# Performance work log

Measured on AMD Instinct MI355X. Metric: run time of the kernel, lower is better.

Reference implementation:

```python
import jax, jax.numpy as jnp
import numpy as np

B, T, C = 2, 2048, 2048
N_HEAD, KV_HEADS = 16, 4
HEAD_DIM = C // N_HEAD  # 128
EPS = 1e-6


def setup_inputs() -> dict:
    key = jax.random.key(0)
    ks = jax.random.split(key, 3)
    x = jax.random.normal(ks[0], (B, T, C), dtype=jnp.float32)
    qkv_out = (N_HEAD + 2 * KV_HEADS) * HEAD_DIM  # 3072
    w_qkv = jax.random.normal(ks[1], (qkv_out, C), dtype=jnp.float32) * 0.02
    w_proj = jax.random.normal(ks[2], (C, C), dtype=jnp.float32) * 0.02
    q_norm_w = jnp.ones((HEAD_DIM,), dtype=jnp.float32)
    k_norm_w = jnp.ones((HEAD_DIM,), dtype=jnp.float32)
    # RoPE frequencies: theta = 10000^{-2i/d}, angles = pos * theta
    inv_freq = 1.0 / (10000.0 ** (np.arange(0, HEAD_DIM, 2, dtype=np.float32) / HEAD_DIM))
    angles = np.arange(T, dtype=np.float32)[:, None] * inv_freq[None, :]  # [T, 64]
    freqs_cos = jnp.asarray(np.cos(angles), dtype=jnp.float32)
    freqs_sin = jnp.asarray(np.sin(angles), dtype=jnp.float32)
    return {"x": x, "w_qkv": w_qkv, "w_proj": w_proj,
            "q_norm_w": q_norm_w, "k_norm_w": k_norm_w,
            "freqs_cos": freqs_cos, "freqs_sin": freqs_sin}


def _rope(t, cos, sin):
    # t: [B, H, T, D]; interpret last dim as D/2 complex pairs (a, b)
    a = t[..., 0::2]
    b = t[..., 1::2]
    oa = a * cos - b * sin
    ob = a * sin + b * cos
    return jnp.stack([oa, ob], axis=-1).reshape(t.shape)


def _rmsnorm(t, w, eps=EPS):
    rms = jnp.sqrt(jnp.mean(t * t, axis=-1, keepdims=True) + eps)
    return w * (t / rms)


def reference(x, w_qkv, w_proj, q_norm_w, k_norm_w, freqs_cos, freqs_sin):
    b, t, c = x.shape
    hd = HEAD_DIM
    qkv = x @ w_qkv.T  # [B, T, 3072]
    q_size = N_HEAD * hd
    kv_size = KV_HEADS * hd
    q = qkv[..., :q_size].reshape(b, t, N_HEAD, hd).transpose(0, 2, 1, 3)
    k = qkv[..., q_size:q_size + kv_size].reshape(b, t, KV_HEADS, hd).transpose(0, 2, 1, 3)
    v = qkv[..., q_size + kv_size:].reshape(b, t, KV_HEADS, hd).transpose(0, 2, 1, 3)
    # repeat_interleave KV heads to match query heads (GQA)
    rep = N_HEAD // KV_HEADS
    k = jnp.repeat(k, rep, axis=1)
    v = jnp.repeat(v, rep, axis=1)
    # RoPE (applied after repeat, matching the torch code order)
    cos = freqs_cos[:t][None, None, :, :]
    sin = freqs_sin[:t][None, None, :, :]
    q = _rope(q, cos, sin)
    k = _rope(k, cos, sin)
    # QK RMSNorm per head_dim
    q = _rmsnorm(q, q_norm_w)
    k = _rmsnorm(k, k_norm_w)
    # causal SDPA
    scores = jnp.einsum('bhqd,bhkd->bhqk', q, k) / jnp.sqrt(jnp.float32(hd))
    causal = jnp.tril(jnp.ones((t, t), dtype=bool))
    scores = jnp.where(causal[None, None], scores, jnp.finfo(scores.dtype).min)
    att = jax.nn.softmax(scores, axis=-1)
    y = jnp.einsum('bhqk,bhkd->bhqd', att, v)
    y = y.transpose(0, 2, 1, 3).reshape(b, t, c)
    return y @ w_proj.T
```

## Files before the change

kernel.cpp:

```cpp
#include <hip/hip_runtime.h>
#include <hip/hip_bf16.h>

#define B_    2
#define T_    2048
#define C_    2048
#define NH_   16
#define KVH_  4
#define HD_   128
#define QKV_  3072
#define M_    4096

typedef float  floatx4 __attribute__((ext_vector_type(4)));
typedef __bf16 bf16x8  __attribute__((ext_vector_type(8)));
typedef __bf16 bf16x4  __attribute__((ext_vector_type(4)));
typedef __bf16 bf16x2  __attribute__((ext_vector_type(2)));

typedef const __attribute__((address_space(1))) void* gas_t;
typedef __attribute__((address_space(3))) void*       las_t;
__device__ __forceinline__ void gl_lds16(const void* g, void* l) {
  __builtin_amdgcn_global_load_lds((gas_t)g, (las_t)l, 16, 0, 0);
}

__global__ __launch_bounds__(256) void cvt_bf16(const float* __restrict__ src,
                                                __bf16* __restrict__ dst, int n4) {
  int i = blockIdx.x * blockDim.x + threadIdx.x;
  if (i < n4) {
    float4 f = ((const float4*)src)[i];
    bf16x4 o = { (__bf16)f.x, (__bf16)f.y, (__bf16)f.z, (__bf16)f.w };
    ((bf16x4*)dst)[i] = o;
  }
}

__global__ __launch_bounds__(256) void gemm_bt(const __bf16* __restrict__ A,
                                               const __bf16* __restrict__ Bm,
                                               float* __restrict__ Cc,
                                               int N, int K) {
  __shared__ __align__(16) __bf16 As[128 * 32];
  __shared__ __align__(16) __bf16 Bs[128 * 32];
  const int tid  = threadIdx.x;
  const int wid  = tid >> 6, lane = tid & 63, quad = lane >> 4, r16 = lane & 15;
  const int bm   = blockIdx.y * 128, bn = blockIdx.x * 128;
  const int wm   = (wid >> 1) * 64, wn = (wid & 1) * 64;
  const int srow = wid * 16 + (lane >> 2);
  const int scol = (lane & 3) * 8;
  const __bf16* aptr = A  + (size_t)(bm + srow) * K + scol;
  const __bf16* bptr = Bm + (size_t)(bn + srow) * K + scol;
  __bf16* ldsA0 = &As[wid * 512];
  __bf16* ldsA1 = &As[2048 + wid * 512];
  __bf16* ldsB0 = &Bs[wid * 512];
  __bf16* ldsB1 = &Bs[2048 + wid * 512];
  const size_t rowskip = (size_t)64 * K;

  floatx4 acc[4][4];
  #pragma unroll
  for (int i = 0; i < 4; i++)
    #pragma unroll
    for (int j = 0; j < 4; j++) acc[i][j] = (floatx4){0.f, 0.f, 0.f, 0.f};

  for (int k0 = 0; k0 < K; k0 += 32) {
    gl_lds16(aptr + k0,           ldsA0);
    gl_lds16(aptr + rowskip + k0, ldsA1);
    gl_lds16(bptr + k0,           ldsB0);
    gl_lds16(bptr + rowskip + k0, ldsB1);
    __syncthreads();

    bf16x8 af[4], bfr[4];
    #pragma unroll
    for (int i = 0; i < 4; i++) af[i]  = *(const bf16x8*)&As[(wm + i * 16 + r16) * 32 + quad * 8];
    #pragma unroll
    for (int j = 0; j < 4; j++) bfr[j] = *(const bf16x8*)&Bs[(wn + j * 16 + r16) * 32 + quad * 8];

    #pragma unroll
    for (int i = 0; i < 4; i++)
      #pragma unroll
      for (int j = 0; j < 4; j++)
        acc[i][j] = __builtin_amdgcn_mfma_f32_16x16x32_bf16(af[i], bfr[j], acc[i][j], 0, 0, 0);
    __syncthreads();
  }

  #pragma unroll
  for (int i = 0; i < 4; i++) {
    #pragma unroll
    for (int reg = 0; reg < 4; reg++) {
      int row = bm + wm + i * 16 + quad * 4 + reg;
      float* crow = Cc + (size_t)row * N + bn + wn;
      #pragma unroll
      for (int j = 0; j < 4; j++) crow[j * 16 + r16] = acc[i][j][reg];
    }
  }
}

__global__ __launch_bounds__(256) void rope_norm(const float* __restrict__ qkv,
                                                 const float* __restrict__ qw,
                                                 const float* __restrict__ kw,
                                                 const float* __restrict__ fc,
                                                 const float* __restrict__ fs,
                                                 __bf16* __restrict__ qn,
                                                 __bf16* __restrict__ kn) {
  const int tid  = threadIdx.x;
  const int wid  = tid >> 6, lane = tid & 63;
  const int row  = blockIdx.x * 4 + wid;
  const int b    = row >> 11, t = row & (T_ - 1);
  const float cs = fc[t * 64 + lane], sn = fs[t * 64 + lane];
  const float* base = qkv + (size_t)row * QKV_;

  #pragma unroll 2
  for (int h = 0; h < NH_; h++) {
    float2 ab = *(const float2*)(base + h * HD_ + 2 * lane);
    float oa = ab.x * cs - ab.y * sn;
    float ob = ab.x * sn + ab.y * cs;
    float ss = oa * oa + ob * ob;
    #pragma unroll
    for (int off = 32; off; off >>= 1) ss += __shfl_xor(ss, off);
    float rinv = rsqrtf(ss * (1.0f / HD_) + 1e-6f);
    bf16x2 o = { (__bf16)(oa * rinv * qw[2 * lane]), (__bf16)(ob * rinv * qw[2 * lane + 1]) };
    *(bf16x2*)&qn[(size_t)((b * NH_ + h) * T_ + t) * HD_ + 2 * lane] = o;
  }
  #pragma unroll 2
  for (int h = 0; h < KVH_; h++) {
    float2 ab = *(const float2*)(base + C_ + h * HD_ + 2 * lane);
    float oa = ab.x * cs - ab.y * sn;
    float ob = ab.x * sn + ab.y * cs;
    float ss = oa * oa + ob * ob;
    #pragma unroll
    for (int off = 32; off; off >>= 1) ss += __shfl_xor(ss, off);
    float rinv = rsqrtf(ss * (1.0f / HD_) + 1e-6f);
    bf16x2 o = { (__bf16)(oa * rinv * kw[2 * lane]), (__bf16)(ob * rinv * kw[2 * lane + 1]) };
    *(bf16x2*)&kn[(size_t)((b * KVH_ + h) * T_ + t) * HD_ + 2 * lane] = o;
  }
}

__global__ __launch_bounds__(256) void vtrans(const float* __restrict__ qkv,
                                              __bf16* __restrict__ vT) {
  __shared__ __bf16 L[64 * 68];
  const int tid = threadIdx.x;
  const int t0 = blockIdx.x * 64;
  const int d0 = blockIdx.y * 64;
  const int z  = blockIdx.z;
  const int b  = z >> 2, hk = z & 3;
  const int srcc = C_ + KVH_ * HD_ + hk * HD_ + d0;
  const int rr = tid >> 4, c4 = (tid & 15) * 4;
  #pragma unroll
  for (int i = 0; i < 4; i++) {
    int t = rr + i * 16;
    float4 f = *(const float4*)&qkv[(size_t)(b * T_ + t0 + t) * QKV_ + srcc + c4];
    bf16x4 o = { (__bf16)f.x, (__bf16)f.y, (__bf16)f.z, (__bf16)f.w };
    *(bf16x4*)&L[t * 68 + c4] = o;
  }
  __syncthreads();
  const int dr = tid >> 3, tc8 = (tid & 7) * 8;
  #pragma unroll
  for (int i = 0; i < 2; i++) {
    int d = dr + i * 32;
    bf16x8 ov;
    #pragma unroll
    for (int j = 0; j < 8; j++) ov[j] = L[(tc8 + j) * 68 + d];
    *(bf16x8*)&vT[(size_t)(z * HD_ + d0 + d) * T_ + t0 + tc8] = ov;
  }
}

__device__ __forceinline__ void kv_prefetch(const __bf16* kbase, const __bf16* vbase,
                                            int kt0, int wid, int lane,
                                            bf16x8 kreg[4], bf16x8 vreg[4]) {
  const int r4 = lane >> 2, c8 = (lane & 3) * 8;
  const __bf16* kg = kbase + (size_t)(kt0 + wid * 16 + r4) * HD_ + c8;
  #pragma unroll
  for (int cb = 0; cb < 4; cb++) kreg[cb] = *(const bf16x8*)(kg + cb * 32);
  #pragma unroll
  for (int s = 0; s < 2; s++) {
    const __bf16* vg = vbase + (size_t)((wid * 2 + s) * 16 + r4) * T_ + kt0 + c8;
    #pragma unroll
    for (int cb = 0; cb < 2; cb++) vreg[s * 2 + cb] = *(const bf16x8*)(vg + cb * 32);
  }
}

__device__ __forceinline__ void kv_commit(__bf16* Ks, __bf16* Vs, int wid, int lane,
                                          const bf16x8 kreg[4], const bf16x8 vreg[4]) {
  #pragma unroll
  for (int cb = 0; cb < 4; cb++)
    *(bf16x8*)(Ks + wid * 2048 + cb * 512 + lane * 8) = kreg[cb];
  #pragma unroll
  for (int s = 0; s < 2; s++)
    #pragma unroll
    for (int cb = 0; cb < 2; cb++)
      *(bf16x8*)(Vs + (wid * 2 + s) * 1024 + cb * 512 + lane * 8) = vreg[s * 2 + cb];
}

__global__ __launch_bounds__(256) void flash(const __bf16* __restrict__ q,
                                             const __bf16* __restrict__ k,
                                             const __bf16* __restrict__ vT,
                                             __bf16* __restrict__ y) {
  __shared__ __align__(16) __bf16 Ks[64 * 128];
  __shared__ __align__(16) __bf16 Vs[128 * 64];
  __shared__ __align__(16) __bf16 Ps[4][16 * 72];
  const int tid = threadIdx.x;
  const int wid = tid >> 6, lane = tid & 63, quad = lane >> 4, r16 = lane & 15;
  const int h = blockIdx.y, b = blockIdx.z;
  const int hk = h >> 2;
  const __bf16* kbase = k  + (size_t)(b * KVH_ + hk) * T_ * HD_;
  const __bf16* vbase = vT + (size_t)(b * KVH_ + hk) * HD_ * T_;
  __bf16* Pw = Ps[wid];
  const float sc = 0.08838834764831845f;
  const float NEG = -__builtin_inff();
  bf16x8 ones;
  #pragma unroll
  for (int i = 0; i < 8; i++) ones[i] = (__bf16)1.0f;

  #pragma unroll 1
  for (int pass = 0; pass < 2; ++pass) {
    const int qt = pass ? blockIdx.x : (31 - blockIdx.x);
    const int nt = qt + 1;
    const int r0 = qt * 64 + wid * 16;

    const __bf16* qrow = q + ((size_t)(b * NH_ + h) * T_ + r0 + r16) * HD_;
    bf16x8 qf[4];
    #pragma unroll
    for (int kb = 0; kb < 4; kb++) qf[kb] = *(const bf16x8*)&qrow[kb * 32 + quad * 8];

    floatx4 o[8], ol = (floatx4){0.f, 0.f, 0.f, 0.f};
    #pragma unroll
    for (int j = 0; j < 8; j++) o[j] = (floatx4){0.f, 0.f, 0.f, 0.f};
    float m_r[4] = {NEG, NEG, NEG, NEG};

    bf16x8 kreg[4], vreg[4];
    kv_prefetch(kbase, vbase, 0, wid, lane, kreg, vreg);

    #pragma unroll 1
    for (int it = 0; it < nt; ++it) {
      __syncthreads();
      kv_commit(Ks, Vs, wid, lane, kreg, vreg);
      __syncthreads();
      if (it + 1 < nt) kv_prefetch(kbase, vbase, (it + 1) * 64, wid, lane, kreg, vreg);

      const int kt0 = it * 64;
      floatx4 s[4];
      #pragma unroll
      for (int cb = 0; cb < 4; cb++) s[cb] = (floatx4){0.f, 0.f, 0.f, 0.f};
      #pragma unroll
      for (int kb = 0; kb < 4; kb++)
        #pragma unroll
        for (int cb = 0; cb < 4; cb++) {
          bf16x8 kf = *(const bf16x8*)&Ks[(cb * 4 + kb) * 512 + r16 * 32 + quad * 8];
          s[cb] = __builtin_amdgcn_mfma_f32_16x16x32_bf16(qf[kb], kf, s[cb], 0, 0, 0);
        }

      const bool last = (it == nt - 1);
      float alpha[4];
      #pragma unroll
      for (int reg = 0; reg < 4; reg++) {
        const int rowq = r0 + quad * 4 + reg;
        float v0 = s[0][reg] * sc, v1 = s[1][reg] * sc, v2 = s[2][reg] * sc, v3 = s[3][reg] * sc;
        if (last) {
          if (kt0 +      r16 > rowq) v0 = NEG;
          if (kt0 + 16 + r16 > rowq) v1 = NEG;
          if (kt0 + 32 + r16 > rowq) v2 = NEG;
          if (kt0 + 48 + r16 > rowq) v3 = NEG;
        }
        float mx = fmaxf(fmaxf(v0, v1), fmaxf(v2, v3));
        #pragma unroll
        for (int off = 8; off; off >>= 1) mx = fmaxf(mx, __shfl_xor(mx, off));
        float mnew = fmaxf(m_r[reg], mx);
        alpha[reg] = __expf(m_r[reg] - mnew);
        m_r[reg] = mnew;
        Pw[(quad * 4 + reg) * 72 +      r16] = (__bf16)__expf(v0 - mnew);
        Pw[(quad * 4 + reg) * 72 + 16 + r16] = (__bf16)__expf(v1 - mnew);
        Pw[(quad * 4 + reg) * 72 + 32 + r16] = (__bf16)__expf(v2 - mnew);
        Pw[(quad * 4 + reg) * 72 + 48 + r16] = (__bf16)__expf(v3 - mnew);
      }
      #pragma unroll
      for (int reg = 0; reg < 4; reg++) {
        ol[reg] *= alpha[reg];
        #pragma unroll
        for (int j = 0; j < 8; j++) o[j][reg] *= alpha[reg];
      }
      __asm__ volatile("" ::: "memory");
      bf16x8 pf0 = *(const bf16x8*)&Pw[r16 * 72 + quad * 8];
      bf16x8 pf1 = *(const bf16x8*)&Pw[r16 * 72 + 32 + quad * 8];
      ol = __builtin_amdgcn_mfma_f32_16x16x32_bf16(pf0, ones, ol, 0, 0, 0);
      ol = __builtin_amdgcn_mfma_f32_16x16x32_bf16(pf1, ones, ol, 0, 0, 0);
      #pragma unroll
      for (int j = 0; j < 8; j++) {
        bf16x8 vf0 = *(const bf16x8*)&Vs[(j * 2 + 0) * 512 + r16 * 32 + quad * 8];
        bf16x8 vf1 = *(const bf16x8*)&Vs[(j * 2 + 1) * 512 + r16 * 32 + quad * 8];
        o[j] = __builtin_amdgcn_mfma_f32_16x16x32_bf16(pf0, vf0, o[j], 0, 0, 0);
        o[j] = __builtin_amdgcn_mfma_f32_16x16x32_bf16(pf1, vf1, o[j], 0, 0, 0);
      }
    }

    #pragma unroll
    for (int reg = 0; reg < 4; reg++) {
      int trow = r0 + quad * 4 + reg;
      float inv = 1.0f / ol[reg];
      __bf16* yr = y + ((size_t)(b * T_) + trow) * C_ + h * HD_;
      #pragma unroll
      for (int j = 0; j < 8; j++) yr[j * 16 + r16] = (__bf16)(o[j][reg] * inv);
    }
  }
}

extern "C" void kernel_launch(void* const* d_in, const int* in_sizes, int n_in,
                              void* d_out, int out_size, void* d_ws, size_t ws_size,
                              hipStream_t stream) {
  const float* x     = (const float*)d_in[0];
  const float* wqkv  = (const float*)d_in[1];
  const float* wproj = (const float*)d_in[2];
  const float* qw    = (const float*)d_in[3];
  const float* kw    = (const float*)d_in[4];
  const float* fc    = (const float*)d_in[5];
  const float* fs    = (const float*)d_in[6];
  float* out = (float*)d_out;

  char* w = (char*)d_ws;
  __bf16* xb     = (__bf16*)w; w += (size_t)M_ * C_ * 2;
  __bf16* wqkvb  = (__bf16*)w; w += (size_t)QKV_ * C_ * 2;
  __bf16* wprojb = (__bf16*)w; w += (size_t)C_ * C_ * 2;
  float*  qkv    = (float*)w;  w += (size_t)M_ * QKV_ * 4;
  __bf16* qn     = (__bf16*)w; w += (size_t)B_ * NH_ * T_ * HD_ * 2;
  __bf16* kn     = (__bf16*)w; w += (size_t)B_ * KVH_ * T_ * HD_ * 2;
  __bf16* vT     = (__bf16*)w; w += (size_t)B_ * KVH_ * T_ * HD_ * 2;
  __bf16* ybf    = (__bf16*)w; w += (size_t)M_ * C_ * 2;

  cvt_bf16<<<M_ * C_ / 4 / 256, 256, 0, stream>>>(x, xb, M_ * C_ / 4);
  cvt_bf16<<<QKV_ * C_ / 4 / 256, 256, 0, stream>>>(wqkv, wqkvb, QKV_ * C_ / 4);
  cvt_bf16<<<C_ * C_ / 4 / 256, 256, 0, stream>>>(wproj, wprojb, C_ * C_ / 4);

  gemm_bt<<<dim3(QKV_ / 128, M_ / 128), 256, 0, stream>>>(xb, wqkvb, qkv, QKV_, C_);
  rope_norm<<<M_ / 4, 256, 0, stream>>>(qkv, qw, kw, fc, fs, qn, kn);
  vtrans<<<dim3(T_ / 64, HD_ / 64, B_ * KVH_), 256, 0, stream>>>(qkv, vT);
  flash<<<dim3(16, NH_, B_), 256, 0, stream>>>(qn, kn, vT, ybf);
  gemm_bt<<<dim3(C_ / 128, M_ / 128), 256, 0, stream>>>(ybf, wprojb, out, C_, C_);
}
```

Baseline: 362.1 us.

## Compute transposed scores in flash attention and pass P through registers

The QK^T MFMA now swaps its operands so each lane holds scores for a single query row across keys. Row max and row sum reduce with two cross-lane shuffles instead of a four-step butterfly per register. The softmax probabilities are packed to bf16 and redistributed with lane shuffles into the PV MFMA operand layout, which removes the per-wave LDS round trip for P and the ones-vector MFMA used for the row sum. The kernel also drops the two-pass pairing of a long and a short query tile per block and launches 32 blocks per head, one query tile each, which gives up the explicit causal load balancing.

```diff
diff --git a/kernel.cpp b/kernel.cpp
--- a/kernel.cpp
+++ b/kernel.cpp
@@ -19,6 +19,11 @@
 typedef __attribute__((address_space(3))) void*       las_t;
 __device__ __forceinline__ void gl_lds16(const void* g, void* l) {
   __builtin_amdgcn_global_load_lds((gas_t)g, (las_t)l, 16, 0, 0);
+}
+
+__device__ __forceinline__ int pack2(float a, float b) {
+  bf16x2 t = { (__bf16)a, (__bf16)b };
+  return __builtin_bit_cast(int, t);
 }
 
 __global__ __launch_bounds__(256) void cvt_bf16(const float* __restrict__ src,
@@ -192,109 +197,128 @@
                                              __bf16* __restrict__ y) {
   __shared__ __align__(16) __bf16 Ks[64 * 128];
   __shared__ __align__(16) __bf16 Vs[128 * 64];
-  __shared__ __align__(16) __bf16 Ps[4][16 * 72];
   const int tid = threadIdx.x;
   const int wid = tid >> 6, lane = tid & 63, quad = lane >> 4, r16 = lane & 15;
   const int h = blockIdx.y, b = blockIdx.z;
   const int hk = h >> 2;
   const __bf16* kbase = k  + (size_t)(b * KVH_ + hk) * T_ * HD_;
   const __bf16* vbase = vT + (size_t)(b * KVH_ + hk) * HD_ * T_;
-  __bf16* Pw = Ps[wid];
   const float sc = 0.08838834764831845f;
   const float NEG = -__builtin_inff();
-  bf16x8 ones;
-  #pragma unroll
-  for (int i = 0; i < 8; i++) ones[i] = (__bf16)1.0f;
+
+  const int qt = 31 - blockIdx.x;
+  const int nt = qt + 1;
+  const int r0 = qt * 64 + wid * 16;
+  const int rowq = r0 + r16;
+
+  const __bf16* qrow = q + ((size_t)(b * NH_ + h) * T_ + r0 + r16) * HD_;
+  bf16x8 qf[4];
+  #pragma unroll
+  for (int kb = 0; kb < 4; kb++) qf[kb] = *(const bf16x8*)&qrow[kb * 32 + quad * 8];
+
+  floatx4 o[8];
+  #pragma unroll
+  for (int j = 0; j < 8; j++) o[j] = (floatx4){0.f, 0.f, 0.f, 0.f};
+  float m_r = NEG, l_r = 0.f;
+
+  bf16x8 kreg[4], vreg[4];
+  kv_prefetch(kbase, vbase, 0, wid, lane, kreg, vreg);
 
   #pragma unroll 1
-  for (int pass = 0; pass < 2; ++pass) {
-    const int qt = pass ? blockIdx.x : (31 - blockIdx.x);
-    const int nt = qt + 1;
-    const int r0 = qt * 64 + wid * 16;
-
-    const __bf16* qrow = q + ((size_t)(b * NH_ + h) * T_ + r0 + r16) * HD_;
-    bf16x8 qf[4];
-    #pragma unroll
-    for (int kb = 0; kb < 4; kb++) qf[kb] = *(const bf16x8*)&qrow[kb * 32 + quad * 8];
-
-    floatx4 o[8], ol = (floatx4){0.f, 0.f, 0.f, 0.f};
-    #pragma unroll
-    for (int j = 0; j < 8; j++) o[j] = (floatx4){0.f, 0.f, 0.f, 0.f};
-    float m_r[4] = {NEG, NEG, NEG, NEG};
-
-    bf16x8 kreg[4], vreg[4];
-    kv_prefetch(kbase, vbase, 0, wid, lane, kreg, vreg);
-
-    #pragma unroll 1
-    for (int it = 0; it < nt; ++it) {
-      __syncthreads();
-      kv_commit(Ks, Vs, wid, lane, kreg, vreg);
-      __syncthreads();
-      if (it + 1 < nt) kv_prefetch(kbase, vbase, (it + 1) * 64, wid, lane, kreg, vreg);
-
-      const int kt0 = it * 64;
-      floatx4 s[4];
-      #pragma unroll
-      for (int cb = 0; cb < 4; cb++) s[cb] = (floatx4){0.f, 0.f, 0.f, 0.f};
-      #pragma unroll
-      for (int kb = 0; kb < 4; kb++)
-        #pragma unroll
-        for (int cb = 0; cb < 4; cb++) {
-          bf16x8 kf = *(const bf16x8*)&Ks[(cb * 4 + kb) * 512 + r16 * 32 + quad * 8];
-          s[cb] = __builtin_amdgcn_mfma_f32_16x16x32_bf16(qf[kb], kf, s[cb], 0, 0, 0);
-        }
-
-      const bool last = (it == nt - 1);
-      float alpha[4];
+  for (int it = 0; it < nt; ++it) {
+    __syncthreads();
+    kv_commit(Ks, Vs, wid, lane, kreg, vreg);
+    __syncthreads();
+    if (it + 1 < nt) kv_prefetch(kbase, vbase, (it + 1) * 64, wid, lane, kreg, vreg);
+
+    const int kt0 = it * 64;
+    floatx4 s[4];
+    #pragma unroll
+    for (int cb = 0; cb < 4; cb++) s[cb] = (floatx4){0.f, 0.f, 0.f, 0.f};
+    #pragma unroll
+    for (int kb = 0; kb < 4; kb++)
+      #pragma unroll
+      for (int cb = 0; cb < 4; cb++) {
+        bf16x8 kf = *(const bf16x8*)&Ks[(cb * 4 + kb) * 512 + r16 * 32 + quad * 8];
+        s[cb] = __builtin_amdgcn_mfma_f32_16x16x32_bf16(kf, qf[kb], s[cb], 0, 0, 0);
+      }
+
+    const bool last = (it == nt - 1);
+    float mx = NEG;
+    #pragma unroll
+    for (int cb = 0; cb < 4; cb++)
       #pragma unroll
       for (int reg = 0; reg < 4; reg++) {
-        const int rowq = r0 + quad * 4 + reg;
-        float v0 = s[0][reg] * sc, v1 = s[1][reg] * sc, v2 = s[2][reg] * sc, v3 = s[3][reg] * sc;
-        if (last) {
-          if (kt0 +      r16 > rowq) v0 = NEG;
-          if (kt0 + 16 + r16 > rowq) v1 = NEG;
-          if (kt0 + 32 + r16 > rowq) v2 = NEG;
-          if (kt0 + 48 + r16 > rowq) v3 = NEG;
-        }
-        float mx = fmaxf(fmaxf(v0, v1), fmaxf(v2, v3));
-        #pragma unroll
-        for (int off = 8; off; off >>= 1) mx = fmaxf(mx, __shfl_xor(mx, off));
-        float mnew = fmaxf(m_r[reg], mx);
-        alpha[reg] = __expf(m_r[reg] - mnew);
-        m_r[reg] = mnew;
-        Pw[(quad * 4 + reg) * 72 +      r16] = (__bf16)__expf(v0 - mnew);
-        Pw[(quad * 4 + reg) * 72 + 16 + r16] = (__bf16)__expf(v1 - mnew);
-        Pw[(quad * 4 + reg) * 72 + 32 + r16] = (__bf16)__expf(v2 - mnew);
-        Pw[(quad * 4 + reg) * 72 + 48 + r16] = (__bf16)__expf(v3 - mnew);
+        float vv = s[cb][reg] * sc;
+        if (last && (kt0 + cb * 16 + quad * 4 + reg > rowq)) vv = NEG;
+        s[cb][reg] = vv;
+        mx = fmaxf(mx, vv);
       }
+    mx = fmaxf(mx, __shfl_xor(mx, 16));
+    mx = fmaxf(mx, __shfl_xor(mx, 32));
+    const float mnew = fmaxf(m_r, mx);
+    const float alpha = __expf(m_r - mnew);
+    m_r = mnew;
+
+    float rs = 0.f;
+    #pragma unroll
+    for (int cb = 0; cb < 4; cb++)
       #pragma unroll
       for (int reg = 0; reg < 4; reg++) {
-        ol[reg] *= alpha[reg];
-        #pragma unroll
-        for (int j = 0; j < 8; j++) o[j][reg] *= alpha[reg];
+        float p = __expf(s[cb][reg] - mnew);
+        s[cb][reg] = p;
+        rs += p;
       }
-      __asm__ volatile("" ::: "memory");
-      bf16x8 pf0 = *(const bf16x8*)&Pw[r16 * 72 + quad * 8];
-      bf16x8 pf1 = *(const bf16x8*)&Pw[r16 * 72 + 32 + quad * 8];
-      ol = __builtin_amdgcn_mfma_f32_16x16x32_bf16(pf0, ones, ol, 0, 0, 0);
-      ol = __builtin_amdgcn_mfma_f32_16x16x32_bf16(pf1, ones, ol, 0, 0, 0);
+    rs += __shfl_xor(rs, 16);
+    rs += __shfl_xor(rs, 32);
+    l_r = l_r * alpha + rs;
+
+    int pk[4][2];
+    #pragma unroll
+    for (int cb = 0; cb < 4; cb++) {
+      pk[cb][0] = pack2(s[cb][0], s[cb][1]);
+      pk[cb][1] = pack2(s[cb][2], s[cb][3]);
+    }
+
+    float al[4];
+    #pragma unroll
+    for (int reg = 0; reg < 4; reg++) al[reg] = __shfl(alpha, quad * 4 + reg);
+    #pragma unroll
+    for (int reg = 0; reg < 4; reg++)
+      #pragma unroll
+      for (int j = 0; j < 8; j++) o[j][reg] *= al[reg];
+
+    const int srcA = ((quad & 1) << 5) + r16;
+    const int srcB = srcA + 16;
+    const bool hi = quad >= 2;
+    #pragma unroll
+    for (int half = 0; half < 2; half++) {
+      const int c0 = half * 2, c1 = half * 2 + 1;
+      int a0 = __shfl(pk[c0][0], srcA), b0 = __shfl(pk[c1][0], srcA);
+      int a1 = __shfl(pk[c0][1], srcA), b1 = __shfl(pk[c1][1], srcA);
+      int a2 = __shfl(pk[c0][0], srcB), b2 = __shfl(pk[c1][0], srcB);
+      int a3 = __shfl(pk[c0][1], srcB), b3 = __shfl(pk[c1][1], srcB);
+      union { int i[4]; bf16x8 v; } u;
+      u.i[0] = hi ? b0 : a0;
+      u.i[1] = hi ? b1 : a1;
+      u.i[2] = hi ? b2 : a2;
+      u.i[3] = hi ? b3 : a3;
       #pragma unroll
       for (int j = 0; j < 8; j++) {
-        bf16x8 vf0 = *(const bf16x8*)&Vs[(j * 2 + 0) * 512 + r16 * 32 + quad * 8];
-        bf16x8 vf1 = *(const bf16x8*)&Vs[(j * 2 + 1) * 512 + r16 * 32 + quad * 8];
-        o[j] = __builtin_amdgcn_mfma_f32_16x16x32_bf16(pf0, vf0, o[j], 0, 0, 0);
-        o[j] = __builtin_amdgcn_mfma_f32_16x16x32_bf16(pf1, vf1, o[j], 0, 0, 0);
+        bf16x8 vf = *(const bf16x8*)&Vs[(j * 2 + half) * 512 + r16 * 32 + quad * 8];
+        o[j] = __builtin_amdgcn_mfma_f32_16x16x32_bf16(u.v, vf, o[j], 0, 0, 0);
       }
     }
-
-    #pragma unroll
-    for (int reg = 0; reg < 4; reg++) {
-      int trow = r0 + quad * 4 + reg;
-      float inv = 1.0f / ol[reg];
-      __bf16* yr = y + ((size_t)(b * T_) + trow) * C_ + h * HD_;
-      #pragma unroll
-      for (int j = 0; j < 8; j++) yr[j * 16 + r16] = (__bf16)(o[j][reg] * inv);
-    }
+  }
+
+  #pragma unroll
+  for (int reg = 0; reg < 4; reg++) {
+    int trow = r0 + quad * 4 + reg;
+    float lf = __shfl(l_r, quad * 4 + reg);
+    float inv = 1.0f / lf;
+    __bf16* yr = y + ((size_t)(b * T_) + trow) * C_ + h * HD_;
+    #pragma unroll
+    for (int j = 0; j < 8; j++) yr[j * 16 + r16] = (__bf16)(o[j][reg] * inv);
   }
 }
 
@@ -327,6 +351,6 @@
   gemm_bt<<<dim3(QKV_ / 128, M_ / 128), 256, 0, stream>>>(xb, wqkvb, qkv, QKV_, C_);
   rope_norm<<<M_ / 4, 256, 0, stream>>>(qkv, qw, kw, fc, fs, qn, kn);
   vtrans<<<dim3(T_ / 64, HD_ / 64, B_ * KVH_), 256, 0, stream>>>(qkv, vT);
-  flash<<<dim3(16, NH_, B_), 256, 0, stream>>>(qn, kn, vT, ybf);
+  flash<<<dim3(32, NH_, B_), 256, 0, stream>>>(qn, kn, vT, ybf);
   gemm_bt<<<dim3(C_ / 128, M_ / 128), 256, 0, stream>>>(ybf, wprojb, out, C_, C_);
 }
```

New measurement: 423.5 us. +16.9%, slower.

## Enlarge flash query tile to 128 rows and double GEMM K-step

Applied to the files above, without the earlier changes.

The flash kernel now has each block handle a 128-row query tile, with each wave owning 32 rows as two 16-row subtiles, so every K/V tile loaded into LDS feeds twice as many MFMAs. The old two-pass balanced scheduling is replaced by a flat 512-block grid that launches the heaviest tiles first and skips fully masked tiles per wave. The GEMM now loads 64 K-columns per barrier pair instead of 32, halving synchronizations. The costs are higher register pressure in flash (launch bounds now ask for 2 blocks), possible warp idling on diagonal tiles, and more LDS use in the GEMM.

```diff
diff --git a/kernel.cpp b/kernel.cpp
--- a/kernel.cpp
+++ b/kernel.cpp
@@ -35,8 +35,8 @@
                                                const __bf16* __restrict__ Bm,
                                                float* __restrict__ Cc,
                                                int N, int K) {
-  __shared__ __align__(16) __bf16 As[128 * 32];
-  __shared__ __align__(16) __bf16 Bs[128 * 32];
+  __shared__ __align__(16) __bf16 As[2][128 * 32];
+  __shared__ __align__(16) __bf16 Bs[2][128 * 32];
   const int tid  = threadIdx.x;
   const int wid  = tid >> 6, lane = tid & 63, quad = lane >> 4, r16 = lane & 15;
   const int bm   = blockIdx.y * 128, bn = blockIdx.x * 128;
@@ -45,10 +45,6 @@
   const int scol = (lane & 3) * 8;
   const __bf16* aptr = A  + (size_t)(bm + srow) * K + scol;
   const __bf16* bptr = Bm + (size_t)(bn + srow) * K + scol;
-  __bf16* ldsA0 = &As[wid * 512];
-  __bf16* ldsA1 = &As[2048 + wid * 512];
-  __bf16* ldsB0 = &Bs[wid * 512];
-  __bf16* ldsB1 = &Bs[2048 + wid * 512];
   const size_t rowskip = (size_t)64 * K;
 
   floatx4 acc[4][4];
@@ -57,24 +53,29 @@
     #pragma unroll
     for (int j = 0; j < 4; j++) acc[i][j] = (floatx4){0.f, 0.f, 0.f, 0.f};
 
-  for (int k0 = 0; k0 < K; k0 += 32) {
-    gl_lds16(aptr + k0,           ldsA0);
-    gl_lds16(aptr + rowskip + k0, ldsA1);
-    gl_lds16(bptr + k0,           ldsB0);
-    gl_lds16(bptr + rowskip + k0, ldsB1);
+  for (int k0 = 0; k0 < K; k0 += 64) {
+    #pragma unroll
+    for (int hf = 0; hf < 2; hf++) {
+      gl_lds16(aptr + k0 + hf * 32,           &As[hf][wid * 512]);
+      gl_lds16(aptr + rowskip + k0 + hf * 32, &As[hf][2048 + wid * 512]);
+      gl_lds16(bptr + k0 + hf * 32,           &Bs[hf][wid * 512]);
+      gl_lds16(bptr + rowskip + k0 + hf * 32, &Bs[hf][2048 + wid * 512]);
+    }
     __syncthreads();
 
-    bf16x8 af[4], bfr[4];
-    #pragma unroll
-    for (int i = 0; i < 4; i++) af[i]  = *(const bf16x8*)&As[(wm + i * 16 + r16) * 32 + quad * 8];
-    #pragma unroll
-    for (int j = 0; j < 4; j++) bfr[j] = *(const bf16x8*)&Bs[(wn + j * 16 + r16) * 32 + quad * 8];
-
-    #pragma unroll
-    for (int i = 0; i < 4; i++)
-      #pragma unroll
-      for (int j = 0; j < 4; j++)
-        acc[i][j] = __builtin_amdgcn_mfma_f32_16x16x32_bf16(af[i], bfr[j], acc[i][j], 0, 0, 0);
+    #pragma unroll
+    for (int hf = 0; hf < 2; hf++) {
+      bf16x8 af[4], bfr[4];
+      #pragma unroll
+      for (int i = 0; i < 4; i++) af[i]  = *(const bf16x8*)&As[hf][(wm + i * 16 + r16) * 32 + quad * 8];
+      #pragma unroll
+      for (int j = 0; j < 4; j++) bfr[j] = *(const bf16x8*)&Bs[hf][(wn + j * 16 + r16) * 32 + quad * 8];
+      #pragma unroll
+      for (int i = 0; i < 4; i++)
+        #pragma unroll
+        for (int j = 0; j < 4; j++)
+          acc[i][j] = __builtin_amdgcn_mfma_f32_16x16x32_bf16(af[i], bfr[j], acc[i][j], 0, 0, 0);
+    }
     __syncthreads();
   }
 
@@ -186,71 +187,85 @@
       *(bf16x8*)(Vs + (wid * 2 + s) * 1024 + cb * 512 + lane * 8) = vreg[s * 2 + cb];
 }
 
-__global__ __launch_bounds__(256) void flash(const __bf16* __restrict__ q,
-                                             const __bf16* __restrict__ k,
-                                             const __bf16* __restrict__ vT,
-                                             __bf16* __restrict__ y) {
+__global__ __launch_bounds__(256, 2) void flash(const __bf16* __restrict__ q,
+                                                const __bf16* __restrict__ k,
+                                                const __bf16* __restrict__ vT,
+                                                __bf16* __restrict__ y) {
   __shared__ __align__(16) __bf16 Ks[64 * 128];
   __shared__ __align__(16) __bf16 Vs[128 * 64];
-  __shared__ __align__(16) __bf16 Ps[4][16 * 72];
+  __shared__ __align__(16) __bf16 Ps[4][2][16 * 72];
   const int tid = threadIdx.x;
   const int wid = tid >> 6, lane = tid & 63, quad = lane >> 4, r16 = lane & 15;
-  const int h = blockIdx.y, b = blockIdx.z;
-  const int hk = h >> 2;
+  const int x   = blockIdx.x;
+  const int qt  = 15 - (x >> 5);
+  const int hl  = x & 31;
+  const int b   = hl >> 4, h = hl & 15, hk = h >> 2;
+  const int nt  = 2 * (qt + 1);
+  const int r0w = qt * 128 + wid * 32;
+
   const __bf16* kbase = k  + (size_t)(b * KVH_ + hk) * T_ * HD_;
   const __bf16* vbase = vT + (size_t)(b * KVH_ + hk) * HD_ * T_;
-  __bf16* Pw = Ps[wid];
   const float sc = 0.08838834764831845f;
   const float NEG = -__builtin_inff();
   bf16x8 ones;
   #pragma unroll
   for (int i = 0; i < 8; i++) ones[i] = (__bf16)1.0f;
 
+  bf16x8 qf[2][4];
+  #pragma unroll
+  for (int s = 0; s < 2; s++) {
+    const __bf16* qrow = q + ((size_t)(b * NH_ + h) * T_ + r0w + s * 16 + r16) * HD_;
+    #pragma unroll
+    for (int kb = 0; kb < 4; kb++) qf[s][kb] = *(const bf16x8*)&qrow[kb * 32 + quad * 8];
+  }
+
+  floatx4 o[2][8], ol[2];
+  #pragma unroll
+  for (int s = 0; s < 2; s++) {
+    ol[s] = (floatx4){0.f, 0.f, 0.f, 0.f};
+    #pragma unroll
+    for (int j = 0; j < 8; j++) o[s][j] = (floatx4){0.f, 0.f, 0.f, 0.f};
+  }
+  float m_r[2][4] = {{NEG, NEG, NEG, NEG}, {NEG, NEG, NEG, NEG}};
+
+  bf16x8 kreg[4], vreg[4];
+  kv_prefetch(kbase, vbase, 0, wid, lane, kreg, vreg);
+
   #pragma unroll 1
-  for (int pass = 0; pass < 2; ++pass) {
-    const int qt = pass ? blockIdx.x : (31 - blockIdx.x);
-    const int nt = qt + 1;
-    const int r0 = qt * 64 + wid * 16;
-
-    const __bf16* qrow = q + ((size_t)(b * NH_ + h) * T_ + r0 + r16) * HD_;
-    bf16x8 qf[4];
-    #pragma unroll
-    for (int kb = 0; kb < 4; kb++) qf[kb] = *(const bf16x8*)&qrow[kb * 32 + quad * 8];
-
-    floatx4 o[8], ol = (floatx4){0.f, 0.f, 0.f, 0.f};
-    #pragma unroll
-    for (int j = 0; j < 8; j++) o[j] = (floatx4){0.f, 0.f, 0.f, 0.f};
-    float m_r[4] = {NEG, NEG, NEG, NEG};
-
-    bf16x8 kreg[4], vreg[4];
-    kv_prefetch(kbase, vbase, 0, wid, lane, kreg, vreg);
-
-    #pragma unroll 1
-    for (int it = 0; it < nt; ++it) {
-      __syncthreads();
-      kv_commit(Ks, Vs, wid, lane, kreg, vreg);
-      __syncthreads();
-      if (it + 1 < nt) kv_prefetch(kbase, vbase, (it + 1) * 64, wid, lane, kreg, vreg);
-
-      const int kt0 = it * 64;
-      floatx4 s[4];
-      #pragma unroll
-      for (int cb = 0; cb < 4; cb++) s[cb] = (floatx4){0.f, 0.f, 0.f, 0.f};
-      #pragma unroll
-      for (int kb = 0; kb < 4; kb++)
-        #pragma unroll
-        for (int cb = 0; cb < 4; cb++) {
-          bf16x8 kf = *(const bf16x8*)&Ks[(cb * 4 + kb) * 512 + r16 * 32 + quad * 8];
-          s[cb] = __builtin_amdgcn_mfma_f32_16x16x32_bf16(qf[kb], kf, s[cb], 0, 0, 0);
-        }
-
-      const bool last = (it == nt - 1);
-      float alpha[4];
+  for (int it = 0; it < nt; ++it) {
+    __syncthreads();
+    kv_commit(Ks, Vs, wid, lane, kreg, vreg);
+    __syncthreads();
+    if (it + 1 < nt) kv_prefetch(kbase, vbase, (it + 1) * 64, wid, lane, kreg, vreg);
+
+    const int kt0 = it * 64;
+    if (kt0 > r0w + 31) continue;
+
+    floatx4 sv[2][4];
+    #pragma unroll
+    for (int s = 0; s < 2; s++)
+      #pragma unroll
+      for (int cb = 0; cb < 4; cb++) sv[s][cb] = (floatx4){0.f, 0.f, 0.f, 0.f};
+    #pragma unroll
+    for (int kb = 0; kb < 4; kb++)
+      #pragma unroll
+      for (int cb = 0; cb < 4; cb++) {
+        bf16x8 kf = *(const bf16x8*)&Ks[(cb * 4 + kb) * 512 + r16 * 32 + quad * 8];
+        sv[0][cb] = __builtin_amdgcn_mfma_f32_16x16x32_bf16(qf[0][kb], kf, sv[0][cb], 0, 0, 0);
+        sv[1][cb] = __builtin_amdgcn_mfma_f32_16x16x32_bf16(qf[1][kb], kf, sv[1][cb], 0, 0, 0);
+      }
+
+    const bool needmask = (kt0 + 64 > r0w);
+    float alpha[2][4];
+    #pragma unroll
+    for (int s = 0; s < 2; s++) {
+      __bf16* Pw = Ps[wid][s];
       #pragma unroll
       for (int reg = 0; reg < 4; reg++) {
-        const int rowq = r0 + quad * 4 + reg;
-        float v0 = s[0][reg] * sc, v1 = s[1][reg] * sc, v2 = s[2][reg] * sc, v3 = s[3][reg] * sc;
-        if (last) {
+        const int rowq = r0w + s * 16 + quad * 4 + reg;
+        float v0 = sv[s][0][reg] * sc, v1 = sv[s][1][reg] * sc;
+        float v2 = sv[s][2][reg] * sc, v3 = sv[s][3][reg] * sc;
+        if (needmask) {
           if (kt0 +      r16 > rowq) v0 = NEG;
           if (kt0 + 16 + r16 > rowq) v1 = NEG;
           if (kt0 + 32 + r16 > rowq) v2 = NEG;
@@ -259,43 +274,53 @@
         float mx = fmaxf(fmaxf(v0, v1), fmaxf(v2, v3));
         #pragma unroll
         for (int off = 8; off; off >>= 1) mx = fmaxf(mx, __shfl_xor(mx, off));
-        float mnew = fmaxf(m_r[reg], mx);
-        alpha[reg] = __expf(m_r[reg] - mnew);
-        m_r[reg] = mnew;
+        float mnew = fmaxf(m_r[s][reg], mx);
+        alpha[s][reg] = __expf(m_r[s][reg] - mnew);
+        m_r[s][reg] = mnew;
         Pw[(quad * 4 + reg) * 72 +      r16] = (__bf16)__expf(v0 - mnew);
         Pw[(quad * 4 + reg) * 72 + 16 + r16] = (__bf16)__expf(v1 - mnew);
         Pw[(quad * 4 + reg) * 72 + 32 + r16] = (__bf16)__expf(v2 - mnew);
         Pw[(quad * 4 + reg) * 72 + 48 + r16] = (__bf16)__expf(v3 - mnew);
       }
+    }
+    #pragma unroll
+    for (int s = 0; s < 2; s++)
       #pragma unroll
       for (int reg = 0; reg < 4; reg++) {
-        ol[reg] *= alpha[reg];
+        ol[s][reg] *= alpha[s][reg];
         #pragma unroll
-        for (int j = 0; j < 8; j++) o[j][reg] *= alpha[reg];
+        for (int j = 0; j < 8; j++) o[s][j][reg] *= alpha[s][reg];
       }
-      __asm__ volatile("" ::: "memory");
-      bf16x8 pf0 = *(const bf16x8*)&Pw[r16 * 72 + quad * 8];
-      bf16x8 pf1 = *(const bf16x8*)&Pw[r16 * 72 + 32 + quad * 8];
-      ol = __builtin_amdgcn_mfma_f32_16x16x32_bf16(pf0, ones, ol, 0, 0, 0);
-      ol = __builtin_amdgcn_mfma_f32_16x16x32_bf16(pf1, ones, ol, 0, 0, 0);
-      #pragma unroll
-      for (int j = 0; j < 8; j++) {
-        bf16x8 vf0 = *(const bf16x8*)&Vs[(j * 2 + 0) * 512 + r16 * 32 + quad * 8];
-        bf16x8 vf1 = *(const bf16x8*)&Vs[(j * 2 + 1) * 512 + r16 * 32 + quad * 8];
-        o[j] = __builtin_amdgcn_mfma_f32_16x16x32_bf16(pf0, vf0, o[j], 0, 0, 0);
-        o[j] = __builtin_amdgcn_mfma_f32_16x16x32_bf16(pf1, vf1, o[j], 0, 0, 0);
-      }
-    }
-
+    __asm__ volatile("" ::: "memory");
+    bf16x8 pf[2][2];
+    #pragma unroll
+    for (int s = 0; s < 2; s++) {
+      pf[s][0] = *(const bf16x8*)&Ps[wid][s][r16 * 72 + quad * 8];
+      pf[s][1] = *(const bf16x8*)&Ps[wid][s][r16 * 72 + 32 + quad * 8];
+      ol[s] = __builtin_amdgcn_mfma_f32_16x16x32_bf16(pf[s][0], ones, ol[s], 0, 0, 0);
+      ol[s] = __builtin_amdgcn_mfma_f32_16x16x32_bf16(pf[s][1], ones, ol[s], 0, 0, 0);
+    }
+    #pragma unroll
+    for (int j = 0; j < 8; j++) {
+      bf16x8 vf0 = *(const bf16x8*)&Vs[(j * 2 + 0) * 512 + r16 * 32 + quad * 8];
+      bf16x8 vf1 = *(const bf16x8*)&Vs[(j * 2 + 1) * 512 + r16 * 32 + quad * 8];
+      o[0][j] = __builtin_amdgcn_mfma_f32_16x16x32_bf16(pf[0][0], vf0, o[0][j], 0, 0, 0);
+      o[0][j] = __builtin_amdgcn_mfma_f32_16x16x32_bf16(pf[0][1], vf1, o[0][j], 0, 0, 0);
+      o[1][j] = __builtin_amdgcn_mfma_f32_16x16x32_bf16(pf[1][0], vf0, o[1][j], 0, 0, 0);
+      o[1][j] = __builtin_amdgcn_mfma_f32_16x16x32_bf16(pf[1][1], vf1, o[1][j], 0, 0, 0);
+    }
+  }
+
+  #pragma unroll
+  for (int s = 0; s < 2; s++)
     #pragma unroll
     for (int reg = 0; reg < 4; reg++) {
-      int trow = r0 + quad * 4 + reg;
-      float inv = 1.0f / ol[reg];
+      int trow = r0w + s * 16 + quad * 4 + reg;
+      float inv = 1.0f / ol[s][reg];
       __bf16* yr = y + ((size_t)(b * T_) + trow) * C_ + h * HD_;
       #pragma unroll
-      for (int j = 0; j < 8; j++) yr[j * 16 + r16] = (__bf16)(o[j][reg] * inv);
-    }
-  }
+      for (int j = 0; j < 8; j++) yr[j * 16 + r16] = (__bf16)(o[s][j][reg] * inv);
+    }
 }
 
 extern "C" void kernel_launch(void* const* d_in, const int* in_sizes, int n_in,
@@ -327,6 +352,6 @@
   gemm_bt<<<dim3(QKV_ / 128, M_ / 128), 256, 0, stream>>>(xb, wqkvb, qkv, QKV_, C_);
   rope_norm<<<M_ / 4, 256, 0, stream>>>(qkv, qw, kw, fc, fs, qn, kn);
   vtrans<<<dim3(T_ / 64, HD_ / 64, B_ * KVH_), 256, 0, stream>>>(qkv, vT);
-  flash<<<dim3(16, NH_, B_), 256, 0, stream>>>(qn, kn, vT, ybf);
+  flash<<<dim3(512), 256, 0, stream>>>(qn, kn, vT, ybf);
   gemm_bt<<<dim3(C_ / 128, M_ / 128), 256, 0, stream>>>(ybf, wprojb, out, C_, C_);
 }
```

Measured after the change: 367.2 us. Within noise of the previous version (+1.4%).
